# Kernel optimization log

Hardware: AMD Instinct MI355X
Metric: run time of the kernel (lower is better)

Reference implementation:

```python
import jax, jax.numpy as jnp
import numpy as np

# Mamba2 defaults (mamba_ssm): expand=2, headdim=64, d_conv=4, ngroups=1
D_MODEL = 1024
D_STATE = 128
INPUT_DIM = 64
NUM_CLASSES = 4
NUM_PATCHES = 16
EXPAND = 2
HEADDIM = 64
D_CONV = 4
D_INNER = EXPAND * D_MODEL          # 2048
NHEADS = D_INNER // HEADDIM         # 32
CONV_DIM = D_INNER + 2 * D_STATE    # x, B, C go through the conv
D_IN_PROJ = 2 * D_INNER + 2 * D_STATE + NHEADS
EPS = 1e-5


def setup_inputs() -> dict:
    key = jax.random.key(0)
    ks = jax.random.split(key, 10)
    B, L = 8, 2048
    s = 0.02
    x = jax.random.normal(ks[0], (B, L, NUM_PATCHES, INPUT_DIM // NUM_PATCHES), jnp.float32)
    return {
        "x": x,
        "w_proj_in": (jax.random.normal(ks[1], (INPUT_DIM, D_MODEL)) * s).astype(jnp.float32),
        "b_proj_in": jnp.zeros((D_MODEL,), jnp.float32),
        "w_in": (jax.random.normal(ks[2], (D_MODEL, D_IN_PROJ)) * s).astype(jnp.float32),
        "conv_w": (jax.random.normal(ks[3], (CONV_DIM, D_CONV)) * s).astype(jnp.float32),
        "conv_b": jnp.zeros((CONV_DIM,), jnp.float32),
        "A_log": jnp.log(jax.random.uniform(ks[4], (NHEADS,), jnp.float32, 1.0, 16.0)),
        "dt_bias": jnp.log(jnp.expm1(jax.random.uniform(ks[5], (NHEADS,), jnp.float32, 1e-3, 0.1))),
        "D": jnp.ones((NHEADS,), jnp.float32),
        "norm_w": jnp.ones((D_INNER,), jnp.float32),
        "w_out": (jax.random.normal(ks[6], (D_INNER, D_MODEL)) * s).astype(jnp.float32),
        "w_head": (jax.random.normal(ks[7], (D_MODEL, NUM_CLASSES * NUM_PATCHES)) * s).astype(jnp.float32),
        "b_head": jnp.zeros((NUM_CLASSES * NUM_PATCHES,), jnp.float32),
    }


def _mamba2(u, w_in, conv_w, conv_b, A_log, dt_bias, D, norm_w, w_out):
    B, L, _ = u.shape
    zxbcdt = u @ w_in                                        # (B,L,D_IN_PROJ)
    z, xBC, dt = jnp.split(zxbcdt, [D_INNER, D_INNER + CONV_DIM], axis=-1)
    # causal depthwise conv1d (kernel D_CONV) + SiLU
    xp = jnp.pad(xBC, ((0, 0), (D_CONV - 1, 0), (0, 0)))
    xc = conv_b + sum(xp[:, k:k + L, :] * conv_w[:, k] for k in range(D_CONV))
    xBC = jax.nn.silu(xc)
    xh, Bm, Cm = jnp.split(xBC, [D_INNER, D_INNER + D_STATE], axis=-1)
    xh = xh.reshape(B, L, NHEADS, HEADDIM)                   # (B,L,H,P)
    dt = jax.nn.softplus(dt + dt_bias)                       # (B,L,H)
    A = -jnp.exp(A_log)                                      # (H,)
    decay = jnp.exp(dt * A)                                  # (B,L,H)

    # selective scan over time; state h: (B,H,N,P)
    def step(h, inp):
        dec, dtk, bk, ck, xk = inp                           # (B,H),(B,H),(B,N),(B,N),(B,H,P)
        h = dec[..., None, None] * h + (dtk[..., None, None] * xk[:, :, None, :]) * bk[:, None, :, None]
        y = jnp.einsum('bhnp,bn->bhp', h, ck)
        return h, y

    xs = (decay.transpose(1, 0, 2), dt.transpose(1, 0, 2),
          Bm.transpose(1, 0, 2), Cm.transpose(1, 0, 2), xh.transpose(1, 0, 2, 3))
    h0 = jnp.zeros((B, NHEADS, D_STATE, HEADDIM), u.dtype)
    _, ys = jax.lax.scan(step, h0, xs)                       # (L,B,H,P)
    y = ys.transpose(1, 0, 2, 3) + D[None, None, :, None] * xh
    y = y.reshape(B, L, D_INNER)
    # gated RMSNorm: norm(y * silu(z)) * weight
    y = y * jax.nn.silu(z)
    y = y * jax.lax.rsqrt(jnp.mean(y * y, axis=-1, keepdims=True) + EPS) * norm_w
    return y @ w_out


def reference(x, w_proj_in, b_proj_in, w_in, conv_w, conv_b, A_log, dt_bias, D, norm_w, w_out, w_head, b_head):
    B, L, P, F = x.shape
    u = x.reshape(B, L, P * F) @ w_proj_in + b_proj_in
    y = _mamba2(u, w_in, conv_w, conv_b, A_log, dt_bias, D, norm_w, w_out)
    logits = y[:, -1, :] @ w_head + b_head
    return logits.reshape(B, NUM_PATCHES, NUM_CLASSES)
```

## Files before the change

### kernel.cpp

```cpp
#include <hip/hip_runtime.h>
#include <hip/hip_bf16.h>
#include <stdint.h>

typedef unsigned short ushort_t;
typedef __attribute__((ext_vector_type(8))) short short8;
typedef __attribute__((ext_vector_type(4))) short short4v;
typedef __attribute__((ext_vector_type(4))) unsigned short ushort4v;
typedef __attribute__((ext_vector_type(4))) float f32x4;

#define L_SEQ   2048
#define BATCH   8
#define M_ROWS  16384
#define EPSV    1e-5f
#define BC_NB   128
#define DTR_NB  1024
#define ZL_NB   256

__device__ __forceinline__ float bf2f(ushort_t u){
  union { uint32_t i; float f; } v; v.i = ((uint32_t)u) << 16; return v.f;
}
__device__ __forceinline__ ushort_t f2bf(float f){
  union { float f; uint32_t i; } v; v.f = f;
  uint32_t r = v.i + 0x7fffu + ((v.i >> 16) & 1u);
  return (ushort_t)(r >> 16);
}

__global__ __launch_bounds__(256)
void k_prep(const float* __restrict__ x, const float* __restrict__ w_proj,
            const float* __restrict__ b_proj, const float* __restrict__ w_in,
            const float* __restrict__ w_out, const float* __restrict__ w_head,
            ushort_t* __restrict__ xb, float* __restrict__ wzT,
            float* __restrict__ wot, float* __restrict__ wht,
            float* __restrict__ wpT, ushort_t* __restrict__ Afold,
            ushort_t* __restrict__ w2tp, float* __restrict__ yfin){
  __shared__ float tile[64][65];
  int bx = blockIdx.x, tid = threadIdx.x;
  if (bx < 4096){
    int i = bx * 256 + tid;
    xb[i] = f2bf(x[i]);
    return;
  }
  bx -= 4096;
  if (bx < 512 + 512 + 16 + 16){
    const float* src; float* dstf;
    int R, C, colOff, j0, k0; bool isWpT = false;
    if (bx < 512){               src = w_in;   dstf = wzT; R = 1024; C = 4384; colOff = 0; j0 = (bx % 32) * 64; k0 = (bx / 32) * 64; }
    else if ((bx -= 512) < 512){ src = w_out;  dstf = wot; R = 2048; C = 1024; colOff = 0; j0 = (bx % 16) * 64; k0 = (bx / 16) * 64; }
    else if ((bx -= 512) < 16){  src = w_head; dstf = wht; R = 1024; C = 64;   colOff = 0; j0 = 0;             k0 = bx * 64; }
    else { bx -= 16;             src = w_proj; dstf = wpT; R = 64;   C = 1024; colOff = 0; j0 = bx * 64;       k0 = 0; isWpT = true; }
    int tx = tid & 63, ty = tid >> 6;
    #pragma unroll
    for (int i = 0; i < 16; ++i){
      int kk = ty * 16 + i;
      if (!isWpT || (k0 + kk) < 64)
        tile[kk][tx] = src[(size_t)(k0 + kk) * C + colOff + j0 + tx];
    }
    __syncthreads();
    #pragma unroll
    for (int i = 0; i < 16; ++i){
      int jj = ty * 16 + i;
      if (isWpT) dstf[(size_t)(j0 + jj) * 64 + tx] = tile[tx][jj];
      else       dstf[(size_t)(j0 + jj) * R + k0 + tx] = tile[tx][jj];
    }
    return;
  }
  bx -= 1056;
  if (bx < 512){
    int i = bx * 256 + tid;
    int row = i >> 10, col = i & 1023;
    float v = (row < 64) ? w_proj[(size_t)row * 1024 + col]
            : (row == 64) ? b_proj[col] : 0.f;
    Afold[i] = f2bf(v);
    return;
  }
  bx -= 512;
  if (bx < 608){
    int j0 = (bx % 38) * 64;
    int k0 = (bx / 38) * 64;
    int tx = tid & 63, ty = tid >> 6;
    #pragma unroll
    for (int i = 0; i < 16; ++i){
      int kk = ty * 16 + i;
      int j = j0 + tx;
      tile[kk][tx] = (j < 2304) ? w_in[(size_t)(k0 + kk) * 4384 + 2048 + j] : 0.f;
    }
    __syncthreads();
    #pragma unroll
    for (int i = 0; i < 16; ++i){
      int jj = ty * 16 + i;
      w2tp[(size_t)(j0 + jj) * 1024 + k0 + tx] = f2bf(tile[tx][jj]);
    }
    return;
  }
  bx -= 608;
  yfin[bx * 256 + tid] = 0.f;
}

__device__ __forceinline__ void gload16(const void* g, void* l){
  __builtin_amdgcn_global_load_lds((const __attribute__((address_space(1))) void*)g,
                                   (__attribute__((address_space(3))) void*)l, 16, 0, 0);
}

__global__ __launch_bounds__(256)
void k_foldg(const ushort_t* __restrict__ Afold, const ushort_t* __restrict__ w2tp,
             ushort_t* __restrict__ Wcb, float* __restrict__ bc,
             const ushort_t* __restrict__ xb, const float* __restrict__ w_proj,
             const float* __restrict__ b_proj, float* __restrict__ ul,
             const float* __restrict__ wpT, const float* __restrict__ w_in,
             float* __restrict__ WdtT, float* __restrict__ bcdt){
  __shared__ ushort_t tA[128 * 32];
  __shared__ ushort_t tB[128 * 32];
  __shared__ float redf[4][64];
  const int bid = blockIdx.x;
  const int tid = threadIdx.x;
  const int lane = tid & 63;
  const int wave = tid >> 6;

  if (bid >= 51){
    int h = bid - 51;
    int a = tid & 63, q = tid >> 6;
    const float* wcol = w_in + 4352 + h;
    float acc = 0.f;
    const int d0 = q * 256;
    for (int d = d0; d < d0 + 256; ++d)
      acc += wpT[(size_t)d * 64 + a] * wcol[(size_t)d * 4384];
    redf[q][a] = acc;
    __syncthreads();
    if (q == 0){
      WdtT[h * 64 + a] = redf[0][a] + redf[1][a] + redf[2][a] + redf[3][a];
      float bacc = 0.f;
      #pragma unroll 4
      for (int i = 0; i < 16; ++i){
        int d = a + 64 * i;
        bacc += b_proj[d] * wcol[(size_t)d * 4384];
      }
      for (int s = 32; s; s >>= 1) bacc += __shfl_down(bacc, s, 64);
      if (a == 0) bcdt[h] = bacc;
    }
    return;
  }

  if (bid >= 19){
    int i = (bid - 19) * 256 + tid;
    int b = i >> 10, d = i & 1023;
    float acc = b_proj[d];
    const ushort_t* xrow = xb + ((size_t)(b * 2048 + 2047)) * 64;
    #pragma unroll 8
    for (int k = 0; k < 64; ++k)
      acc += bf2f(xrow[k]) * w_proj[(size_t)k * 1024 + d];
    ul[b * 1024 + d] = acc;
    return;
  }

  const int n0 = bid * 128;
  const int wr = wave >> 1, wc = wave & 1;
  const int l15 = lane & 15, l4 = lane >> 4;
  const int srow  = lane >> 2;
  const int skoff = (lane & 3) * 8;

  f32x4 acc[4][4];
  #pragma unroll
  for (int m = 0; m < 4; ++m)
    #pragma unroll
    for (int n = 0; n < 4; ++n)
      #pragma unroll
      for (int r = 0; r < 4; ++r) acc[m][n][r] = 0.f;

  for (int k0 = 0; k0 < 1024; k0 += 32){
    #pragma unroll
    for (int r = 0; r < 2; ++r){
      int chunk = r * 4 + wave;
      int rr = chunk * 16 + srow;
      gload16(Afold + (size_t)rr * 1024 + k0 + skoff, &tA[chunk * 512]);
      gload16(w2tp  + (size_t)(n0 + rr) * 1024 + k0 + skoff, &tB[chunk * 512]);
    }
    __syncthreads();
    short8 af[4], bfv[4];
    #pragma unroll
    for (int m = 0; m < 4; ++m)
      af[m] = *(const short8*)&tA[(wr * 64 + m * 16 + l15) * 32 + l4 * 8];
    #pragma unroll
    for (int n = 0; n < 4; ++n)
      bfv[n] = *(const short8*)&tB[(wc * 64 + n * 16 + l15) * 32 + l4 * 8];
    #pragma unroll
    for (int m = 0; m < 4; ++m)
      #pragma unroll
      for (int n = 0; n < 4; ++n)
        acc[m][n] = __builtin_amdgcn_mfma_f32_16x16x32_bf16(af[m], bfv[n], acc[m][n], 0, 0, 0);
    __syncthreads();
  }
  #pragma unroll
  for (int n = 0; n < 4; ++n){
    int col = n0 + wc * 64 + n * 16 + l15;
    #pragma unroll
    for (int m = 0; m < 4; ++m){
      int rowb = wr * 64 + m * 16 + l4 * 4;
      #pragma unroll
      for (int r = 0; r < 4; ++r){
        int row = rowb + r;
        if (row < 64)       Wcb[(size_t)col * 64 + row] = f2bf(acc[m][n][r]);
        else if (row == 64) bc[col] = acc[m][n][r];
      }
    }
  }
}

__global__ __launch_bounds__(512)
void k_gemmBC(const ushort_t* __restrict__ A, const ushort_t* __restrict__ Wcb,
              const float* __restrict__ bc, ushort_t* __restrict__ CBC,
              const float* __restrict__ WdtT, const float* __restrict__ bcdt,
              float* __restrict__ dtr, const float* __restrict__ ul,
              const float* __restrict__ wzT, float* __restrict__ z_last){
  __shared__ ushort_t lds[24576];
  const int bid = blockIdx.x;
  const int tid = threadIdx.x;
  const int lane = tid & 63;
  const int wave = tid >> 6;

  if (bid >= BC_NB + DTR_NB){
    int col = (bid - BC_NB - DTR_NB) * 8 + wave;
    float acc[8] = {0.f, 0.f, 0.f, 0.f, 0.f, 0.f, 0.f, 0.f};
    const float* wp = wzT + (size_t)col * 1024;
    #pragma unroll 4
    for (int i = 0; i < 16; ++i){
      int k = i * 64 + lane;
      float w = wp[k];
      #pragma unroll
      for (int b = 0; b < 8; ++b)
        acc[b] += ul[b * 1024 + k] * w;
    }
    #pragma unroll
    for (int b = 0; b < 8; ++b){
      float v = acc[b];
      for (int s = 32; s; s >>= 1) v += __shfl_down(v, s, 64);
      if (lane == 0) z_last[b * 2048 + col] = v;
    }
    return;
  }

  if (bid >= BC_NB){
    int r = tid >> 5, h = tid & 31;
    size_t m = (size_t)(bid - BC_NB) * 16 + r;
    const ushort_t* xrow = A + m * 64;
    const float* wrow = WdtT + h * 64;
    float acc = bcdt[h];
    #pragma unroll 8
    for (int k = 0; k < 64; ++k)
      acc += bf2f(xrow[k]) * wrow[k];
    dtr[m * 32 + h] = acc;
    return;
  }

  const int cpx = BC_NB >> 3;
  const int swz = (bid & 7) * cpx + (bid >> 3);
  const int m0 = (swz >> 1) * 256, n0 = (swz & 1) * 128;
  const int l15 = lane & 15, l4 = lane >> 4;

  #pragma unroll
  for (int i = 0; i < 4; ++i){
    int idx = i * 512 + tid;
    int row = idx >> 3, c16 = idx & 7;
    int scol = (c16 * 8) ^ ((row & 7) << 3);
    gload16(A + (size_t)(m0 + row) * 64 + scol, &lds[idx * 8]);
  }
  #pragma unroll
  for (int i = 0; i < 2; ++i){
    int idx = i * 512 + tid;
    int row = idx >> 3, c16 = idx & 7;
    int scol = (c16 * 8) ^ ((row & 7) << 3);
    gload16(Wcb + (size_t)(2048 + n0 + row) * 64 + scol, &lds[16384 + idx * 8]);
  }
  __syncthreads();

  f32x4 acc[2][8];
  #pragma unroll
  for (int m = 0; m < 2; ++m)
    #pragma unroll
    for (int n = 0; n < 8; ++n)
      #pragma unroll
      for (int r = 0; r < 4; ++r) acc[m][n][r] = 0.f;

  #pragma unroll
  for (int kk = 0; kk < 2; ++kk){
    short8 af[2], bfv[8];
    #pragma unroll
    for (int m = 0; m < 2; ++m){
      int row = wave * 32 + m * 16 + l15;
      int e = (kk * 32 + l4 * 8) ^ ((row & 7) << 3);
      af[m] = *(const short8*)&lds[row * 64 + e];
    }
    #pragma unroll
    for (int n = 0; n < 8; ++n){
      int row = n * 16 + l15;
      int e = (kk * 32 + l4 * 8) ^ ((row & 7) << 3);
      bfv[n] = *(const short8*)&lds[16384 + row * 64 + e];
    }
    #pragma unroll
    for (int m = 0; m < 2; ++m)
      #pragma unroll
      for (int n = 0; n < 8; ++n)
        acc[m][n] = __builtin_amdgcn_mfma_f32_16x16x32_bf16(af[m], bfv[n], acc[m][n], 0, 0, 0);
  }
  __syncthreads();

  #pragma unroll
  for (int half = 0; half < 2; ++half){
    if ((wave >> 2) == half){
      int wl = wave & 3;
      #pragma unroll
      for (int n = 0; n < 8; ++n){
        int col = n * 16 + l15;
        float bv = bc[2048 + n0 + col];
        #pragma unroll
        for (int m = 0; m < 2; ++m){
          #pragma unroll
          for (int r = 0; r < 4; ++r){
            int lr = wl * 32 + m * 16 + l4 * 4 + r;
            lds[lr * 128 + (col ^ ((lr & 7) << 3))] = f2bf(acc[m][n][r] + bv);
          }
        }
      }
    }
    __syncthreads();
    #pragma unroll
    for (int p = 0; p < 4; ++p){
      int gr = p * 32 + (tid >> 4);
      int cg = (tid & 15) * 8;
      short8 v = *(const short8*)&lds[gr * 128 + (cg ^ ((gr & 7) << 3))];
      *(short8*)&CBC[(size_t)(m0 + half * 128 + gr) * 256 + n0 + cg] = v;
    }
    __syncthreads();
  }
}

__global__ __launch_bounds__(256)
void k_bcg2(const ushort_t* __restrict__ xbcBC, const float* __restrict__ conv_w,
            const float* __restrict__ conv_b, float* __restrict__ g){
  __shared__ float csh[128];
  __shared__ float wsh[128][4];
  __shared__ float bsh[128];
  const int b = blockIdx.y;
  const int t0 = blockIdx.x * 32;
  const int tid = threadIdx.x;
  const size_t rowb = (size_t)b * 2048;

  if (tid < 128){
    int cB = 2048 + tid;
    f32x4 wb = *(const f32x4*)&conv_w[cB * 4];
    #pragma unroll
    for (int k = 0; k < 4; ++k) wsh[tid][k] = wb[k];
    bsh[tid] = conv_b[cB];
    int c = 2176 + tid;
    f32x4 w4 = *(const f32x4*)&conv_w[c * 4];
    float a = conv_b[c];
    #pragma unroll
    for (int k = 0; k < 4; ++k)
      a += bf2f(xbcBC[(rowb + 2044 + k) * 256 + 128 + tid]) * w4[k];
    csh[tid] = a / (1.f + __expf(-a));
  }
  __syncthreads();

  const int t = t0 + (tid >> 3);
  const int lg = tid & 7;
  const int cb0 = lg * 16;
  short8 v0[4], v1[4];
  #pragma unroll
  for (int k = 0; k < 4; ++k){
    int tt = t - 3 + k;
    if (tt >= 0){
      v0[k] = *(const short8*)&xbcBC[(rowb + tt) * 256 + cb0];
      v1[k] = *(const short8*)&xbcBC[(rowb + tt) * 256 + cb0 + 8];
    } else {
      short8 z = {0,0,0,0,0,0,0,0}; v0[k] = z; v1[k] = z;
    }
  }
  float gacc = 0.f;
  #pragma unroll
  for (int j = 0; j < 8; ++j){
    int c = cb0 + j;
    float a = bsh[c];
    #pragma unroll
    for (int k = 0; k < 4; ++k) a += bf2f((ushort_t)v0[k][j]) * wsh[c][k];
    gacc += (a / (1.f + __expf(-a))) * csh[c];
  }
  #pragma unroll
  for (int j = 0; j < 8; ++j){
    int c = cb0 + 8 + j;
    float a = bsh[c];
    #pragma unroll
    for (int k = 0; k < 4; ++k) a += bf2f((ushort_t)v1[k][j]) * wsh[c][k];
    gacc += (a / (1.f + __expf(-a))) * csh[c];
  }
  #pragma unroll
  for (int s = 4; s; s >>= 1) gacc += __shfl_down(gacc, s, 8);
  if (lg == 0) g[rowb + t] = gacc;
}

__global__ void k_coeff(const float* __restrict__ dt_raw, const float* __restrict__ dt_bias,
                        const float* __restrict__ A_log, const float* __restrict__ g,
                        float* __restrict__ coeffw){
  __shared__ float csum[256];
  int bh = blockIdx.x;
  int b = bh >> 5, h = bh & 31;
  float Ah = -__expf(A_log[h]);
  float bias = dt_bias[h];
  int tid = threadIdx.x;
  size_t base = (size_t)b * 2048;
  float d[8], dts[8];
  #pragma unroll
  for (int j = 0; j < 8; ++j){
    int t = tid * 8 + j;
    float x = dt_raw[(base + t) * 32 + h] + bias;
    float sp = (x > 20.f) ? x : log1pf(__expf(x));
    dts[j] = sp;
    d[j] = sp * Ah;
  }
  float cs = 0.f;
  #pragma unroll
  for (int j = 0; j < 8; ++j) cs += d[j];
  csum[tid] = cs;
  __syncthreads();
  float suf = 0.f;
  for (int j = tid + 1; j < 256; ++j) suf += csum[j];
  float S = suf, outv[8];
  for (int j = 7; j >= 0; --j){ outv[j] = S; S += d[j]; }
  #pragma unroll
  for (int j = 0; j < 8; ++j){
    int t = tid * 8 + j;
    coeffw[(size_t)bh * 2048 + t] = __expf(outv[j]) * dts[j] * g[base + t];
  }
}

__global__ __launch_bounds__(512)
void k_xsum(const ushort_t* __restrict__ xb, const ushort_t* __restrict__ Wcb,
            const float* __restrict__ bcv, const float* __restrict__ conv_w,
            const float* __restrict__ conv_b, const float* __restrict__ cfw,
            float* __restrict__ yfin, ushort_t* __restrict__ xhl){
  __shared__ char S[32768];
  ushort_t* Al = (ushort_t*)S;
  ushort_t* Ol = (ushort_t*)(S + 10240);
  float*    Cl = (float*)(S + 30720);
  const int tid = threadIdx.x, lane = tid & 63, wave = tid >> 6;
  const int n0 = blockIdx.x * 128;
  const int mt = blockIdx.y;
  const int b = mt >> 3, t0 = (mt & 7) * 256;
  const int l15 = lane & 15, l4 = lane >> 4;

  const int colw = wave * 16 + l15;
  const short8 bf0 = *(const short8*)&Wcb[(size_t)(n0 + colw) * 64 + l4 * 8];
  const short8 bf1 = *(const short8*)&Wcb[(size_t)(n0 + colw) * 64 + 32 + l4 * 8];
  const float bcw = bcv[n0 + colw];

  {
    int h2 = tid >> 8, t = tid & 255;
    Cl[h2 * 256 + t] = cfw[((size_t)(b * 32 + (n0 >> 6) + h2)) * 2048 + t0 + t];
  }
  const int g = tid & 15, sl = tid >> 4;
  float wv[8][4], cb8[8];
  #pragma unroll
  for (int j = 0; j < 8; ++j){
    int c = n0 + g * 8 + j;
    f32x4 w4 = *(const f32x4*)&conv_w[c * 4];
    #pragma unroll
    for (int k = 0; k < 4; ++k) wv[j][k] = w4[k];
    cb8[j] = conv_b[c];
  }
  float accS[8] = {0.f, 0.f, 0.f, 0.f, 0.f, 0.f, 0.f, 0.f};
  float silL[8];
  #pragma unroll
  for (int j = 0; j < 8; ++j) silL[j] = 0.f;

  #pragma unroll
  for (int i = 0; i < 2; ++i){
    int idx = i * 512 + tid;
    if (idx < 640){
      int row = idx >> 3, c16 = idx & 7;
      int gt = t0 - 16 + row;
      if (gt < 0) gt = 0;
      int scol = (c16 * 8) ^ ((row & 7) << 3);
      gload16(xb + ((size_t)b * 2048 + gt) * 64 + scol, &Al[idx * 8]);
    }
  }

  for (int q = 0; q < 4; ++q){
    asm volatile("s_waitcnt vmcnt(0)" ::: "memory");
    __syncthreads();
    #pragma unroll
    for (int rt = 0; rt < 5; ++rt){
      f32x4 acc = {0.f, 0.f, 0.f, 0.f};
      int arow = rt * 16 + l15;
      int ae0 = (l4 * 8) ^ ((arow & 7) << 3);
      int ae1 = (32 + l4 * 8) ^ ((arow & 7) << 3);
      short8 af0 = *(const short8*)&Al[arow * 64 + ae0];
      short8 af1 = *(const short8*)&Al[arow * 64 + ae1];
      acc = __builtin_amdgcn_mfma_f32_16x16x32_bf16(af0, bf0, acc, 0, 0, 0);
      acc = __builtin_amdgcn_mfma_f32_16x16x32_bf16(af1, bf1, acc, 0, 0, 0);
      #pragma unroll
      for (int r = 0; r < 4; ++r){
        int lr = rt * 16 + l4 * 4 + r;
        Ol[lr * 128 + (colw ^ ((lr & 7) << 3))] = f2bf(acc[r] + bcw);
      }
    }
    __syncthreads();
    if (q < 3){
      const int tq = t0 + (q + 1) * 64;
      #pragma unroll
      for (int i = 0; i < 2; ++i){
        int idx = i * 512 + tid;
        if (idx < 640){
          int row = idx >> 3, c16 = idx & 7;
          int gt = tq - 16 + row;
          int scol = (c16 * 8) ^ ((row & 7) << 3);
          gload16(xb + ((size_t)b * 2048 + gt) * 64 + scol, &Al[idx * 8]);
        }
      }
    }
    if (q == 0 && t0 == 0){
      for (int i = tid; i < 2048; i += 512) Ol[i] = 0;
      __syncthreads();
    }
    {
      const int base = sl * 2;
      float r0[8], r1[8], r2[8], r3[8];
      #pragma unroll
      for (int i = 0; i < 3; ++i){
        int lr = 16 + base - 3 + i;
        int e = (g * 8) ^ ((lr & 7) << 3);
        short8 v = *(const short8*)&Ol[lr * 128 + e];
        float* dst = (i == 0) ? r0 : (i == 1) ? r1 : r2;
        #pragma unroll
        for (int j = 0; j < 8; ++j) dst[j] = bf2f((ushort_t)v[j]);
      }
      #pragma unroll
      for (int d2 = 0; d2 < 2; ++d2){
        int lr = 16 + base + d2;
        int e = (g * 8) ^ ((lr & 7) << 3);
        short8 v = *(const short8*)&Ol[lr * 128 + e];
        #pragma unroll
        for (int j = 0; j < 8; ++j) r3[j] = bf2f((ushort_t)v[j]);
        float cf = Cl[(g >> 3) * 256 + q * 64 + base + d2];
        #pragma unroll
        for (int j = 0; j < 8; ++j){
          float a = cb8[j] + r0[j] * wv[j][0] + r1[j] * wv[j][1]
                  + r2[j] * wv[j][2] + r3[j] * wv[j][3];
          float s_ = a / (1.f + __expf(-a));
          accS[j] += cf * s_;
          silL[j] = s_;
        }
        #pragma unroll
        for (int j = 0; j < 8; ++j){ r0[j] = r1[j]; r1[j] = r2[j]; r2[j] = r3[j]; }
      }
    }
  }
  __syncthreads();
  if ((mt & 7) == 7 && sl == 31){
    ushort4v s0, s1;
    #pragma unroll
    for (int j = 0; j < 4; ++j){ s0[j] = f2bf(silL[j]); s1[j] = f2bf(silL[4 + j]); }
    *(ushort4v*)&xhl[b * 2048 + n0 + g * 8] = s0;
    *(ushort4v*)&xhl[b * 2048 + n0 + g * 8 + 4] = s1;
  }
  float* red = (float*)S;
  #pragma unroll
  for (int j = 0; j < 8; ++j) red[sl * 128 + g * 8 + j] = accS[j];
  __syncthreads();
  if (tid < 128){
    float v = 0.f;
    #pragma unroll 8
    for (int s2 = 0; s2 < 32; ++s2) v += red[s2 * 128 + tid];
    atomicAdd(&yfin[b * 2048 + n0 + tid], v);
  }
}

__global__ void k_norm(const float* __restrict__ yfin, const ushort_t* __restrict__ xhl,
                       const float* __restrict__ Dp, const float* __restrict__ z_last,
                       const float* __restrict__ norm_w, float* __restrict__ yn){
  __shared__ float red[256];
  int b = blockIdx.x, tid = threadIdx.x;
  float vals[8], ss = 0.f;
  #pragma unroll
  for (int j = 0; j < 8; ++j){
    int c = tid + 256 * j;
    float v = yfin[b * 2048 + c] + Dp[c >> 6] * bf2f(xhl[b * 2048 + c]);
    float z = z_last[b * 2048 + c];
    float yg = v * (z / (1.f + __expf(-z)));
    vals[j] = yg; ss += yg * yg;
  }
  red[tid] = ss; __syncthreads();
  for (int s = 128; s; s >>= 1){
    if (tid < s) red[tid] += red[tid + s];
    __syncthreads();
  }
  float scale = rsqrtf(red[0] / 2048.f + EPSV);
  #pragma unroll
  for (int j = 0; j < 8; ++j){
    int c = tid + 256 * j;
    yn[b * 2048 + c] = vals[j] * scale * norm_w[c];
  }
}

__global__ __launch_bounds__(64)
void k_outproj(const float* __restrict__ yn, const float* __restrict__ wot,
               float* __restrict__ o){
  int col = blockIdx.x;
  int l = threadIdx.x;
  float acc[8] = {0.f, 0.f, 0.f, 0.f, 0.f, 0.f, 0.f, 0.f};
  const float* wp = wot + (size_t)col * 2048;
  #pragma unroll 4
  for (int i = 0; i < 32; ++i){
    int k = i * 64 + l;
    float w = wp[k];
    #pragma unroll
    for (int b = 0; b < 8; ++b)
      acc[b] += yn[b * 2048 + k] * w;
  }
  #pragma unroll
  for (int b = 0; b < 8; ++b){
    float v = acc[b];
    for (int s = 32; s; s >>= 1) v += __shfl_down(v, s, 64);
    if (l == 0) o[b * 1024 + col] = v;
  }
}

__global__ __launch_bounds__(64)
void k_head(const float* __restrict__ o, const float* __restrict__ wht,
            const float* __restrict__ b_head, float* __restrict__ out){
  int j = blockIdx.x;
  int l = threadIdx.x;
  float acc[8] = {0.f, 0.f, 0.f, 0.f, 0.f, 0.f, 0.f, 0.f};
  const float* wp = wht + (size_t)j * 1024;
  #pragma unroll 4
  for (int i = 0; i < 16; ++i){
    int k = i * 64 + l;
    float w = wp[k];
    #pragma unroll
    for (int b = 0; b < 8; ++b)
      acc[b] += o[b * 1024 + k] * w;
  }
  #pragma unroll
  for (int b = 0; b < 8; ++b){
    float v = acc[b];
    for (int s = 32; s; s >>= 1) v += __shfl_down(v, s, 64);
    if (l == 0) out[b * 64 + j] = v + b_head[j];
  }
}

extern "C" void kernel_launch(void* const* d_in, const int* in_sizes, int n_in,
                              void* d_out, int out_size, void* d_ws, size_t ws_size,
                              hipStream_t stream){
  (void)in_sizes; (void)n_in; (void)out_size; (void)ws_size;
  const float* x       = (const float*)d_in[0];
  const float* w_proj  = (const float*)d_in[1];
  const float* b_proj  = (const float*)d_in[2];
  const float* w_in    = (const float*)d_in[3];
  const float* conv_w  = (const float*)d_in[4];
  const float* conv_b  = (const float*)d_in[5];
  const float* A_log   = (const float*)d_in[6];
  const float* dt_bias = (const float*)d_in[7];
  const float* Dp      = (const float*)d_in[8];
  const float* norm_w  = (const float*)d_in[9];
  const float* w_out   = (const float*)d_in[10];
  const float* w_head  = (const float*)d_in[11];
  const float* b_head  = (const float*)d_in[12];
  float* out = (float*)d_out;

  char* ws = (char*)d_ws;
  size_t off = 0;
  auto alloc = [&](size_t bytes)->char*{
    char* p = ws + off; off += (bytes + 255) & ~(size_t)255; return p;
  };
  ushort_t* xb    = (ushort_t*)alloc((size_t)M_ROWS * 64 * 2);
  float*    wzT   = (float*)alloc((size_t)2048 * 1024 * 4);
  float*    wot   = (float*)alloc((size_t)1024 * 2048 * 4);
  float*    wht   = (float*)alloc((size_t)64 * 1024 * 4);
  float*    wpT   = (float*)alloc((size_t)1024 * 64 * 4);
  ushort_t* Afold = (ushort_t*)alloc((size_t)128 * 1024 * 2);
  ushort_t* w2tp  = (ushort_t*)alloc((size_t)2432 * 1024 * 2);
  ushort_t* Wcb   = (ushort_t*)alloc((size_t)2432 * 64 * 2);
  float*    bcv   = (float*)alloc((size_t)2432 * 4);
  float*    WdtT  = (float*)alloc((size_t)32 * 64 * 4);
  float*    bcdt  = (float*)alloc((size_t)32 * 4);
  float*    ul    = (float*)alloc((size_t)8 * 1024 * 4);
  ushort_t* xbcBC = (ushort_t*)alloc((size_t)M_ROWS * 256 * 2);
  float*    dtr   = (float*)alloc((size_t)M_ROWS * 32 * 4);
  float*    g     = (float*)alloc((size_t)M_ROWS * 4);
  float*    cfw   = (float*)alloc((size_t)256 * 2048 * 4);
  ushort_t* xhl   = (ushort_t*)alloc((size_t)8 * 2048 * 2);
  float*    yfin  = (float*)alloc((size_t)8 * 2048 * 4);
  float*    zl    = (float*)alloc((size_t)8 * 2048 * 4);
  float*    yn    = (float*)alloc((size_t)8 * 2048 * 4);
  float*    ov    = (float*)alloc((size_t)8 * 1024 * 4);

  k_prep<<<4096 + 512 + 512 + 16 + 16 + 512 + 608 + 64, 256, 0, stream>>>(
      x, w_proj, b_proj, w_in, w_out, w_head, xb, wzT, wot, wht, wpT, Afold, w2tp, yfin);

  k_foldg<<<19 + 32 + 32, 256, 0, stream>>>(Afold, w2tp, Wcb, bcv, xb, w_proj, b_proj, ul,
                                            wpT, w_in, WdtT, bcdt);

  k_gemmBC<<<BC_NB + DTR_NB + ZL_NB, 512, 0, stream>>>(
      xb, Wcb, bcv, xbcBC, WdtT, bcdt, dtr, ul, wzT, zl);

  dim3 gbc(64, 8);
  k_bcg2<<<gbc, 256, 0, stream>>>(xbcBC, conv_w, conv_b, g);

  k_coeff<<<256, 256, 0, stream>>>(dtr, dt_bias, A_log, g, cfw);

  dim3 gx(16, 64);
  k_xsum<<<gx, 512, 0, stream>>>(xb, Wcb, bcv, conv_w, conv_b, cfw, yfin, xhl);

  k_norm<<<8, 256, 0, stream>>>(yfin, xhl, Dp, zl, norm_w, yn);
  k_outproj<<<1024, 64, 0, stream>>>(yn, wot, ov);
  k_head<<<64, 64, 0, stream>>>(ov, wht, b_head, out);
}
```

Measured before the change: 141.5 us.

## Compute causal conv directly from MFMA registers via cross-lane shuffles

The k_xsum kernel no longer writes the MFMA projection output to shared memory as bf16 and re-reads it for the depthwise conv. Each lane now keeps its accumulator fragment in registers, fetches the three preceding timesteps with wave shuffles, and applies conv, SiLU and the C-weighted sum in place. The block-wide reduction through LDS is replaced by two xor-shuffles, which cuts LDS use from 32KB to 12KB and removes barriers. The conv inputs now stay in fp32 instead of being rounded to bf16, which changes numerics slightly. The shuffle boundary logic for the first timestep is also new and could be wrong.

Measured after the change: 134.1 us, median of 2. 1.06x faster.

```diff
diff --git a/kernel.cpp b/kernel.cpp
--- a/kernel.cpp
+++ b/kernel.cpp
@@ -436,10 +436,9 @@
             const float* __restrict__ bcv, const float* __restrict__ conv_w,
             const float* __restrict__ conv_b, const float* __restrict__ cfw,
             float* __restrict__ yfin, ushort_t* __restrict__ xhl){
-  __shared__ char S[32768];
+  __shared__ char S[12288];
   ushort_t* Al = (ushort_t*)S;
-  ushort_t* Ol = (ushort_t*)(S + 10240);
-  float*    Cl = (float*)(S + 30720);
+  float*    Cl = (float*)(S + 10240);
   const int tid = threadIdx.x, lane = tid & 63, wave = tid >> 6;
   const int n0 = blockIdx.x * 128;
   const int mt = blockIdx.y;
@@ -450,25 +449,17 @@
   const short8 bf0 = *(const short8*)&Wcb[(size_t)(n0 + colw) * 64 + l4 * 8];
   const short8 bf1 = *(const short8*)&Wcb[(size_t)(n0 + colw) * 64 + 32 + l4 * 8];
   const float bcw = bcv[n0 + colw];
+  const f32x4 wcv = *(const f32x4*)&conv_w[(n0 + colw) * 4];
+  const float cbw = conv_b[n0 + colw];
+  const int hsel = (colw >> 6);
 
   {
     int h2 = tid >> 8, t = tid & 255;
     Cl[h2 * 256 + t] = cfw[((size_t)(b * 32 + (n0 >> 6) + h2)) * 2048 + t0 + t];
   }
-  const int g = tid & 15, sl = tid >> 4;
-  float wv[8][4], cb8[8];
-  #pragma unroll
-  for (int j = 0; j < 8; ++j){
-    int c = n0 + g * 8 + j;
-    f32x4 w4 = *(const f32x4*)&conv_w[c * 4];
-    #pragma unroll
-    for (int k = 0; k < 4; ++k) wv[j][k] = w4[k];
-    cb8[j] = conv_b[c];
-  }
-  float accS[8] = {0.f, 0.f, 0.f, 0.f, 0.f, 0.f, 0.f, 0.f};
-  float silL[8];
-  #pragma unroll
-  for (int j = 0; j < 8; ++j) silL[j] = 0.f;
+
+  float accS = 0.f;
+  float silLast = 0.f;
 
   #pragma unroll
   for (int i = 0; i < 2; ++i){
@@ -485,6 +476,7 @@
   for (int q = 0; q < 4; ++q){
     asm volatile("s_waitcnt vmcnt(0)" ::: "memory");
     __syncthreads();
+    f32x4 aa[5];
     #pragma unroll
     for (int rt = 0; rt < 5; ++rt){
       f32x4 acc = {0.f, 0.f, 0.f, 0.f};
@@ -496,10 +488,7 @@
       acc = __builtin_amdgcn_mfma_f32_16x16x32_bf16(af0, bf0, acc, 0, 0, 0);
       acc = __builtin_amdgcn_mfma_f32_16x16x32_bf16(af1, bf1, acc, 0, 0, 0);
       #pragma unroll
-      for (int r = 0; r < 4; ++r){
-        int lr = rt * 16 + l4 * 4 + r;
-        Ol[lr * 128 + (colw ^ ((lr & 7) << 3))] = f2bf(acc[r] + bcw);
-      }
+      for (int r = 0; r < 4; ++r) aa[rt][r] = acc[r] + bcw;
     }
     __syncthreads();
     if (q < 3){
@@ -515,61 +504,43 @@
         }
       }
     }
-    if (q == 0 && t0 == 0){
-      for (int i = tid; i < 2048; i += 512) Ol[i] = 0;
-      __syncthreads();
-    }
-    {
-      const int base = sl * 2;
-      float r0[8], r1[8], r2[8], r3[8];
-      #pragma unroll
-      for (int i = 0; i < 3; ++i){
-        int lr = 16 + base - 3 + i;
-        int e = (g * 8) ^ ((lr & 7) << 3);
-        short8 v = *(const short8*)&Ol[lr * 128 + e];
-        float* dst = (i == 0) ? r0 : (i == 1) ? r1 : r2;
-        #pragma unroll
-        for (int j = 0; j < 8; ++j) dst[j] = bf2f((ushort_t)v[j]);
+    #pragma unroll
+    for (int rt = 1; rt < 5; ++rt){
+      float P1, P2, P3;
+      {
+        float u1 = __shfl_up(aa[rt][1], 16, 64);
+        float u2 = __shfl_up(aa[rt][2], 16, 64);
+        float u3 = __shfl_up(aa[rt][3], 16, 64);
+        float v1 = __shfl(aa[rt - 1][1], l15 + 48, 64);
+        float v2 = __shfl(aa[rt - 1][2], l15 + 48, 64);
+        float v3 = __shfl(aa[rt - 1][3], l15 + 48, 64);
+        bool lo = (l4 == 0);
+        P1 = lo ? v1 : u1;
+        P2 = lo ? v2 : u2;
+        P3 = lo ? v3 : u3;
+        if (t0 == 0 && q == 0 && rt == 1 && lo){ P1 = 0.f; P2 = 0.f; P3 = 0.f; }
       }
-      #pragma unroll
-      for (int d2 = 0; d2 < 2; ++d2){
-        int lr = 16 + base + d2;
-        int e = (g * 8) ^ ((lr & 7) << 3);
-        short8 v = *(const short8*)&Ol[lr * 128 + e];
-        #pragma unroll
-        for (int j = 0; j < 8; ++j) r3[j] = bf2f((ushort_t)v[j]);
-        float cf = Cl[(g >> 3) * 256 + q * 64 + base + d2];
-        #pragma unroll
-        for (int j = 0; j < 8; ++j){
-          float a = cb8[j] + r0[j] * wv[j][0] + r1[j] * wv[j][1]
-                  + r2[j] * wv[j][2] + r3[j] * wv[j][3];
-          float s_ = a / (1.f + __expf(-a));
-          accS[j] += cf * s_;
-          silL[j] = s_;
-        }
-        #pragma unroll
-        for (int j = 0; j < 8; ++j){ r0[j] = r1[j]; r1[j] = r2[j]; r2[j] = r3[j]; }
-      }
-    }
-  }
-  __syncthreads();
-  if ((mt & 7) == 7 && sl == 31){
-    ushort4v s0, s1;
-    #pragma unroll
-    for (int j = 0; j < 4; ++j){ s0[j] = f2bf(silL[j]); s1[j] = f2bf(silL[4 + j]); }
-    *(ushort4v*)&xhl[b * 2048 + n0 + g * 8] = s0;
-    *(ushort4v*)&xhl[b * 2048 + n0 + g * 8 + 4] = s1;
-  }
-  float* red = (float*)S;
-  #pragma unroll
-  for (int j = 0; j < 8; ++j) red[sl * 128 + g * 8 + j] = accS[j];
-  __syncthreads();
-  if (tid < 128){
-    float v = 0.f;
-    #pragma unroll 8
-    for (int s2 = 0; s2 < 32; ++s2) v += red[s2 * 128 + tid];
-    atomicAdd(&yfin[b * 2048 + n0 + tid], v);
-  }
+      float x0 = aa[rt][0], x1 = aa[rt][1], x2 = aa[rt][2], x3 = aa[rt][3];
+      float o0 = cbw + wcv[0] * P1 + wcv[1] * P2 + wcv[2] * P3 + wcv[3] * x0;
+      float o1 = cbw + wcv[0] * P2 + wcv[1] * P3 + wcv[2] * x0 + wcv[3] * x1;
+      float o2 = cbw + wcv[0] * P3 + wcv[1] * x0 + wcv[2] * x1 + wcv[3] * x2;
+      float o3 = cbw + wcv[0] * x0 + wcv[1] * x1 + wcv[2] * x2 + wcv[3] * x3;
+      float s0 = o0 / (1.f + __expf(-o0));
+      float s1 = o1 / (1.f + __expf(-o1));
+      float s2 = o2 / (1.f + __expf(-o2));
+      float s3 = o3 / (1.f + __expf(-o3));
+      const int tb = q * 64 + (rt - 1) * 16 + l4 * 4;
+      const float* cfp = &Cl[hsel * 256 + tb];
+      accS += cfp[0] * s0 + cfp[1] * s1 + cfp[2] * s2 + cfp[3] * s3;
+      if (q == 3 && rt == 4) silLast = s3;
+    }
+  }
+  if ((mt & 7) == 7 && l4 == 3)
+    xhl[b * 2048 + n0 + colw] = f2bf(silLast);
+  accS += __shfl_xor(accS, 16, 64);
+  accS += __shfl_xor(accS, 32, 64);
+  if (l4 == 0)
+    atomicAdd(&yfin[b * 2048 + n0 + colw], accS);
 }
 
 __global__ void k_norm(const float* __restrict__ yfin, const ushort_t* __restrict__ xhl,
```
